# Kernel tuning notes

Measured on AMD Instinct MI355X. Metric: run time of the kernel, lower is better.

The kernel has to match this reference:

```python
import jax, jax.numpy as jnp
import numpy as np

BLOCK = 64  # block_size from config
NEG_INF = -1e9


def setup_inputs() -> dict:
    key = jax.random.key(0)
    k1, k2, k3, k4 = jax.random.split(key, 4)
    B, H, S, D = 2, 8, 2048, 64
    nb = S // BLOCK  # 32 blocks per side
    query = jax.random.normal(k1, (B, H, S, D), dtype=jnp.float32)
    key_t = jax.random.normal(k2, (B, H, S, D), dtype=jnp.float32)
    value = jax.random.normal(k3, (B, H, S, D), dtype=jnp.float32)
    # binary block mask; force diagonal blocks on so every row has >=1 valid key
    mat = jax.random.randint(k4, (nb, nb), 0, 2).astype(jnp.int32)
    mat = mat.at[jnp.arange(nb), jnp.arange(nb)].set(1)
    mask = jnp.ones((B, S), dtype=jnp.float32)  # padding mask (1 = keep)
    return {"query": query, "key": key_t, "value": value, "mask": mask, "mat": mat}


def reference(query, key, value, mask, mat):
    # Upsample block mask [nb, nb] -> dense [S, S] (nearest, like nn.Upsample)
    block_dense = jnp.repeat(jnp.repeat(mat, BLOCK, axis=0), BLOCK, axis=1) > 0
    # Block-sparse QK^T: only positions inside nonzero blocks participate.
    scores = jnp.einsum('bhqd,bhkd->bhqk', query, key)
    # Additive padding-mask bias, as in the original: 1e6 * (1 - mask)
    scores = scores - 1e6 * (1.0 - mask)[:, None, None, :]
    # Positions outside the block pattern are excluded from the softmax.
    scores = jnp.where(block_dense[None, None, :, :], scores, NEG_INF)
    attn = jax.nn.softmax(scores, axis=-1)
    out = jnp.einsum('bhqk,bhkd->bhqd', attn, value)
    return out
```

## Files before the change

### kernel.cpp

```cpp
#include <hip/hip_runtime.h>


typedef __attribute__((ext_vector_type(8))) short short8;
typedef __attribute__((ext_vector_type(4))) short short4_;
typedef __attribute__((ext_vector_type(4))) float float4_;

#define B_   2
#define H_   8
#define S_   2048
#define D_   64
#define NB_  32
#define KP   72

__device__ __forceinline__ short f2bf(float f) {
    union { float f; unsigned int u; } x; x.f = f;
    unsigned int r = x.u + 0x7FFFu + ((x.u >> 16) & 1u);
    return (short)(r >> 16);
}
__device__ __forceinline__ float bf2f(short s) {
    union { unsigned int u; float f; } x; x.u = ((unsigned int)(unsigned short)s) << 16;
    return x.f;
}

__global__ __launch_bounds__(256)
void preconvert_kernel(const float* __restrict__ K, const float* __restrict__ V,
                       short* __restrict__ Khi, short* __restrict__ Klo,
                       short* __restrict__ Vt) {
    __shared__ short vn[64 * KP];
    const int tid = threadIdx.x;
    const int kt  = blockIdx.x;
    const int bh  = blockIdx.y;
    const size_t tb = ((size_t)bh * S_ + kt * 64) * D_;

#pragma unroll
    for (int it = 0; it < 4; ++it) {
        int i = tid + it * 256;
        int row = i >> 4, c4 = (i & 15) * 4;
        float4_ kv = *(const float4_*)(K + tb + row * D_ + c4);
        short4_ hi, lo;
#pragma unroll
        for (int e = 0; e < 4; ++e) {
            hi[e] = f2bf(kv[e]);
            lo[e] = f2bf(kv[e] - bf2f(hi[e]));
        }
        *(short4_*)(Khi + tb + row * D_ + c4) = hi;
        *(short4_*)(Klo + tb + row * D_ + c4) = lo;
        float4_ vv = *(const float4_*)(V + tb + row * D_ + c4);
        short4_ vb;
#pragma unroll
        for (int e = 0; e < 4; ++e) vb[e] = f2bf(vv[e]);
        *(short4_*)&vn[row * KP + c4] = vb;
    }
    __syncthreads();
#pragma unroll
    for (int it = 0; it < 2; ++it) {
        int i = tid + it * 256;
        int rowd = i >> 3, key8 = (i & 7) * 8;
        short8 o;
#pragma unroll
        for (int e = 0; e < 8; ++e) o[e] = vn[(key8 + e) * KP + rowd];
        *(short8*)(Vt + ((size_t)bh * D_ + rowd) * S_ + kt * 64 + key8) = o;
    }
}

__global__ __launch_bounds__(256, 2)
void blockmask_attn_mfma(const float* __restrict__ Q,
                         const float* __restrict__ K,
                         const float* __restrict__ V,
                         const float* __restrict__ Msk,
                         const int* __restrict__ Mat,
                         float* __restrict__ O,
                         const short* __restrict__ Khi_g,
                         const short* __restrict__ Klo_g,
                         const short* __restrict__ Vt_g,
                         int use_pre) {
    __shared__ __align__(16) short lds[4 * 64 * KP];
    short* Khi = lds;
    short* Klo = lds + 64 * KP;
    short* Vt  = lds + 2 * 64 * KP;
    short* Pl  = lds + 3 * 64 * KP;

    const int tid  = threadIdx.x;
    const int wave = tid >> 6;
    const int lane = tid & 63;
    const int c    = lane & 15;
    const int quad = lane >> 4;

    const int qb = blockIdx.x;
    const int bh = blockIdx.y;
    const int b  = bh / H_;
    const size_t base = (size_t)bh * S_ * D_;

    short8 qh0, qh1, ql0, ql1;
    {
        const float* qp = Q + base + (size_t)(qb * 64 + wave * 16 + c) * D_ + quad * 8;
#pragma unroll
        for (int e = 0; e < 8; ++e) {
            float f0 = qp[e], f1 = qp[e + 32];
            qh0[e] = f2bf(f0); ql0[e] = f2bf(f0 - bf2f(qh0[e]));
            qh1[e] = f2bf(f1); ql1[e] = f2bf(f1 - bf2f(qh1[e]));
        }
    }

    float4_ o[4];
    float l_part[4];
#pragma unroll
    for (int t = 0; t < 4; ++t) { o[t][0] = 0.f; o[t][1] = 0.f; o[t][2] = 0.f; o[t][3] = 0.f; }
#pragma unroll
    for (int j = 0; j < 4; ++j) l_part[j] = 0.f;

    for (int kb = 0; kb < NB_; ++kb) {
        if (Mat[qb * NB_ + kb] == 0) continue;

        __syncthreads();
        if (use_pre) {
            const short* kh = Khi_g + base + (size_t)kb * 64 * D_;
            const short* kl = Klo_g + base + (size_t)kb * 64 * D_;
            const short* vt = Vt_g + (size_t)bh * D_ * S_ + kb * 64;
#pragma unroll
            for (int it = 0; it < 2; ++it) {
                int i = tid + it * 256;
                int row = i >> 3, col8 = (i & 7) * 8;
                *(short8*)&Khi[row * KP + col8] = *(const short8*)(kh + row * D_ + col8);
                *(short8*)&Klo[row * KP + col8] = *(const short8*)(kl + row * D_ + col8);
                *(short8*)&Vt[row * KP + col8]  = *(const short8*)(vt + (size_t)row * S_ + col8);
            }
        } else {
            const float* kg = K + base + (size_t)kb * 64 * D_;
            const float* vg = V + base + (size_t)kb * 64 * D_;
#pragma unroll
            for (int it = 0; it < 4; ++it) {
                int i = tid + it * 256;
                int row = i >> 4, c4 = (i & 15) * 4;
                float4_ kv = *(const float4_*)(kg + row * D_ + c4);
                short4_ hi, lo;
#pragma unroll
                for (int e = 0; e < 4; ++e) {
                    hi[e] = f2bf(kv[e]);
                    lo[e] = f2bf(kv[e] - bf2f(hi[e]));
                }
                *(short4_*)&Khi[row * KP + c4] = hi;
                *(short4_*)&Klo[row * KP + c4] = lo;
                float4_ vv = *(const float4_*)(vg + row * D_ + c4);
#pragma unroll
                for (int e = 0; e < 4; ++e) Vt[(c4 + e) * KP + row] = f2bf(vv[e]);
            }
        }
        __syncthreads();

        float4_ sc[4];
#pragma unroll
        for (int t = 0; t < 4; ++t) { sc[t][0] = 0.f; sc[t][1] = 0.f; sc[t][2] = 0.f; sc[t][3] = 0.f; }
#pragma unroll
        for (int t = 0; t < 4; ++t) {
            const short* kph = &Khi[(t * 16 + c) * KP + quad * 8];
            const short* kpl = &Klo[(t * 16 + c) * KP + quad * 8];
            short8 kh0 = *(const short8*)(kph);
            short8 kh1 = *(const short8*)(kph + 32);
            short8 kl0 = *(const short8*)(kpl);
            short8 kl1 = *(const short8*)(kpl + 32);
            sc[t] = __builtin_amdgcn_mfma_f32_16x16x32_bf16(qh0, kh0, sc[t], 0, 0, 0);
            sc[t] = __builtin_amdgcn_mfma_f32_16x16x32_bf16(qh1, kh1, sc[t], 0, 0, 0);
            sc[t] = __builtin_amdgcn_mfma_f32_16x16x32_bf16(qh0, kl0, sc[t], 0, 0, 0);
            sc[t] = __builtin_amdgcn_mfma_f32_16x16x32_bf16(qh1, kl1, sc[t], 0, 0, 0);
            sc[t] = __builtin_amdgcn_mfma_f32_16x16x32_bf16(ql0, kh0, sc[t], 0, 0, 0);
            sc[t] = __builtin_amdgcn_mfma_f32_16x16x32_bf16(ql1, kh1, sc[t], 0, 0, 0);
        }

        short* Pw = Pl + wave * 16 * KP;
#pragma unroll
        for (int t = 0; t < 4; ++t) {
            float bias = -1.0e6f * (1.0f - Msk[(size_t)b * S_ + kb * 64 + t * 16 + c]);
#pragma unroll
            for (int j = 0; j < 4; ++j) {
                float p = __expf(sc[t][j] + bias);
                l_part[j] += p;
                Pw[(quad * 4 + j) * KP + t * 16 + c] = f2bf(p);
            }
        }

        const short* pp = Pl + wave * 16 * KP + c * KP + quad * 8;
        short8 pa0 = *(const short8*)(pp);
        short8 pa1 = *(const short8*)(pp + 32);

#pragma unroll
        for (int t = 0; t < 4; ++t) {
            const short* vp = &Vt[(t * 16 + c) * KP + quad * 8];
            short8 vb0 = *(const short8*)(vp);
            short8 vb1 = *(const short8*)(vp + 32);
            o[t] = __builtin_amdgcn_mfma_f32_16x16x32_bf16(pa0, vb0, o[t], 0, 0, 0);
            o[t] = __builtin_amdgcn_mfma_f32_16x16x32_bf16(pa1, vb1, o[t], 0, 0, 0);
        }
    }

#pragma unroll
    for (int j = 0; j < 4; ++j) {
        float rs = l_part[j];
        rs += __shfl_xor(rs, 1);
        rs += __shfl_xor(rs, 2);
        rs += __shfl_xor(rs, 4);
        rs += __shfl_xor(rs, 8);
        float inv = 1.0f / rs;
        size_t rowoff = base + (size_t)(qb * 64 + wave * 16 + quad * 4 + j) * D_;
#pragma unroll
        for (int t = 0; t < 4; ++t)
            O[rowoff + t * 16 + c] = o[t][j] * inv;
    }
}

extern "C" void kernel_launch(void* const* d_in, const int* in_sizes, int n_in,
                              void* d_out, int out_size, void* d_ws, size_t ws_size,
                              hipStream_t stream) {
    const float* q   = (const float*)d_in[0];
    const float* k   = (const float*)d_in[1];
    const float* v   = (const float*)d_in[2];
    const float* msk = (const float*)d_in[3];
    const int*   mat = (const int*)d_in[4];
    float*       out = (float*)d_out;

    const size_t elems = (size_t)B_ * H_ * S_ * D_;
    const size_t need  = 3 * elems * sizeof(short);
    int use_pre = (ws_size >= need) ? 1 : 0;

    short* khi = (short*)d_ws;
    short* klo = khi + elems;
    short* vt  = klo + elems;

    dim3 grid(NB_, B_ * H_);
    dim3 block(256);
    if (use_pre)
        preconvert_kernel<<<grid, block, 0, stream>>>(k, v, khi, klo, vt);
    blockmask_attn_mfma<<<grid, block, 0, stream>>>(q, k, v, msk, mat, out,
                                                    khi, klo, vt, use_pre);
}
```

Baseline: 124.9 us.

## Use one-wave blocks loading K/V fragments directly from global, skipping LDS staging

Adds a new attention kernel where each 64-thread block handles 16 query rows and loads K-hi/K-lo/V-transposed fragments straight from global memory into registers, with no LDS staging and no block barriers. It also stores V transposed per 64-key tile so each tile is contiguous, and walks the nonzero blocks with a ballot bitmask instead of testing every block. This removes the __syncthreads and LDS copy overhead and raises block count, but the same K/V data is now fetched from global (through cache) by four times as many blocks, raising cache traffic and register pressure.

```diff
diff --git a/kernel.cpp b/kernel.cpp
--- a/kernel.cpp
+++ b/kernel.cpp
@@ -25,7 +25,7 @@
 __global__ __launch_bounds__(256)
 void preconvert_kernel(const float* __restrict__ K, const float* __restrict__ V,
                        short* __restrict__ Khi, short* __restrict__ Klo,
-                       short* __restrict__ Vt) {
+                       short* __restrict__ Vtb) {
     __shared__ short vn[64 * KP];
     const int tid = threadIdx.x;
     const int kt  = blockIdx.x;
@@ -59,21 +59,129 @@
         short8 o;
 #pragma unroll
         for (int e = 0; e < 8; ++e) o[e] = vn[(key8 + e) * KP + rowd];
-        *(short8*)(Vt + ((size_t)bh * D_ + rowd) * S_ + kt * 64 + key8) = o;
+        *(short8*)(Vtb + (((size_t)(bh * NB_ + kt)) * 64 + rowd) * 64 + key8) = o;
+    }
+}
+
+__global__ __launch_bounds__(64, 2)
+void attn_mfma_nb(const float* __restrict__ Q,
+                  const float* __restrict__ Msk,
+                  const int* __restrict__ Mat,
+                  float* __restrict__ O,
+                  const short* __restrict__ Khi_g,
+                  const short* __restrict__ Klo_g,
+                  const short* __restrict__ Vtb_g) {
+    __shared__ __align__(16) short Pl[16 * KP];
+
+    const int lane = threadIdx.x & 63;
+    const int c    = lane & 15;
+    const int quad = lane >> 4;
+
+    const int qt = blockIdx.x;
+    const int bh = blockIdx.y;
+    const int b  = bh / H_;
+    const int qb = qt >> 2;
+    const size_t base = (size_t)bh * S_ * D_;
+
+    short8 qh0, qh1, ql0, ql1;
+    {
+        const float* qp = Q + base + (size_t)(qt * 16 + c) * D_ + quad * 8;
+#pragma unroll
+        for (int e = 0; e < 8; ++e) {
+            float f0 = qp[e], f1 = qp[e + 32];
+            qh0[e] = f2bf(f0); ql0[e] = f2bf(f0 - bf2f(qh0[e]));
+            qh1[e] = f2bf(f1); ql1[e] = f2bf(f1 - bf2f(qh1[e]));
+        }
+    }
+
+    float4_ o[4];
+    float l_part[4];
+#pragma unroll
+    for (int t = 0; t < 4; ++t) { o[t][0] = 0.f; o[t][1] = 0.f; o[t][2] = 0.f; o[t][3] = 0.f; }
+#pragma unroll
+    for (int j = 0; j < 4; ++j) l_part[j] = 0.f;
+
+    unsigned long long bm = __ballot(Mat[qb * NB_ + (lane & 31)] != 0);
+    unsigned int mbits = (unsigned int)(bm & 0xFFFFFFFFull);
+
+    while (mbits) {
+        const int kb = __builtin_ctz(mbits);
+        mbits &= mbits - 1;
+
+        const short* kh = Khi_g + base + (size_t)kb * 64 * D_;
+        const short* kl = Klo_g + base + (size_t)kb * 64 * D_;
+        const short* vt = Vtb_g + ((size_t)(bh * NB_ + kb)) * 64 * 64;
+
+        short8 KH0[4], KH1[4], KL0[4], KL1[4], VB0[4], VB1[4];
+        float biasv[4];
+#pragma unroll
+        for (int t = 0; t < 4; ++t) {
+            const int off = (t * 16 + c) * 64 + quad * 8;
+            VB0[t] = *(const short8*)(vt + off);
+            VB1[t] = *(const short8*)(vt + off + 32);
+            KH0[t] = *(const short8*)(kh + off);
+            KH1[t] = *(const short8*)(kh + off + 32);
+            KL0[t] = *(const short8*)(kl + off);
+            KL1[t] = *(const short8*)(kl + off + 32);
+            biasv[t] = -1.0e6f * (1.0f - Msk[(size_t)b * S_ + kb * 64 + t * 16 + c]);
+        }
+
+        float4_ sc[4];
+#pragma unroll
+        for (int t = 0; t < 4; ++t) { sc[t][0] = 0.f; sc[t][1] = 0.f; sc[t][2] = 0.f; sc[t][3] = 0.f; }
+#pragma unroll
+        for (int t = 0; t < 4; ++t) {
+            sc[t] = __builtin_amdgcn_mfma_f32_16x16x32_bf16(qh0, KH0[t], sc[t], 0, 0, 0);
+            sc[t] = __builtin_amdgcn_mfma_f32_16x16x32_bf16(qh1, KH1[t], sc[t], 0, 0, 0);
+            sc[t] = __builtin_amdgcn_mfma_f32_16x16x32_bf16(qh0, KL0[t], sc[t], 0, 0, 0);
+            sc[t] = __builtin_amdgcn_mfma_f32_16x16x32_bf16(qh1, KL1[t], sc[t], 0, 0, 0);
+            sc[t] = __builtin_amdgcn_mfma_f32_16x16x32_bf16(ql0, KH0[t], sc[t], 0, 0, 0);
+            sc[t] = __builtin_amdgcn_mfma_f32_16x16x32_bf16(ql1, KH1[t], sc[t], 0, 0, 0);
+        }
+
+#pragma unroll
+        for (int t = 0; t < 4; ++t) {
+#pragma unroll
+            for (int j = 0; j < 4; ++j) {
+                float p = __expf(sc[t][j] + biasv[t]);
+                l_part[j] += p;
+                Pl[(quad * 4 + j) * KP + t * 16 + c] = f2bf(p);
+            }
+        }
+
+        const short* pp = Pl + c * KP + quad * 8;
+        short8 pa0 = *(const short8*)(pp);
+        short8 pa1 = *(const short8*)(pp + 32);
+
+#pragma unroll
+        for (int t = 0; t < 4; ++t) {
+            o[t] = __builtin_amdgcn_mfma_f32_16x16x32_bf16(pa0, VB0[t], o[t], 0, 0, 0);
+            o[t] = __builtin_amdgcn_mfma_f32_16x16x32_bf16(pa1, VB1[t], o[t], 0, 0, 0);
+        }
+    }
+
+#pragma unroll
+    for (int j = 0; j < 4; ++j) {
+        float rs = l_part[j];
+        rs += __shfl_xor(rs, 1);
+        rs += __shfl_xor(rs, 2);
+        rs += __shfl_xor(rs, 4);
+        rs += __shfl_xor(rs, 8);
+        float inv = 1.0f / rs;
+        size_t rowoff = base + (size_t)(qt * 16 + quad * 4 + j) * D_;
+#pragma unroll
+        for (int t = 0; t < 4; ++t)
+            O[rowoff + t * 16 + c] = o[t][j] * inv;
     }
 }
 
 __global__ __launch_bounds__(256, 2)
-void blockmask_attn_mfma(const float* __restrict__ Q,
-                         const float* __restrict__ K,
-                         const float* __restrict__ V,
-                         const float* __restrict__ Msk,
-                         const int* __restrict__ Mat,
-                         float* __restrict__ O,
-                         const short* __restrict__ Khi_g,
-                         const short* __restrict__ Klo_g,
-                         const short* __restrict__ Vt_g,
-                         int use_pre) {
+void attn_mfma_fb(const float* __restrict__ Q,
+                  const float* __restrict__ K,
+                  const float* __restrict__ V,
+                  const float* __restrict__ Msk,
+                  const int* __restrict__ Mat,
+                  float* __restrict__ O) {
     __shared__ __align__(16) short lds[4 * 64 * KP];
     short* Khi = lds;
     short* Klo = lds + 64 * KP;
@@ -113,19 +221,7 @@
         if (Mat[qb * NB_ + kb] == 0) continue;
 
         __syncthreads();
-        if (use_pre) {
-            const short* kh = Khi_g + base + (size_t)kb * 64 * D_;
-            const short* kl = Klo_g + base + (size_t)kb * 64 * D_;
-            const short* vt = Vt_g + (size_t)bh * D_ * S_ + kb * 64;
-#pragma unroll
-            for (int it = 0; it < 2; ++it) {
-                int i = tid + it * 256;
-                int row = i >> 3, col8 = (i & 7) * 8;
-                *(short8*)&Khi[row * KP + col8] = *(const short8*)(kh + row * D_ + col8);
-                *(short8*)&Klo[row * KP + col8] = *(const short8*)(kl + row * D_ + col8);
-                *(short8*)&Vt[row * KP + col8]  = *(const short8*)(vt + (size_t)row * S_ + col8);
-            }
-        } else {
+        {
             const float* kg = K + base + (size_t)kb * 64 * D_;
             const float* vg = V + base + (size_t)kb * 64 * D_;
 #pragma unroll
@@ -220,16 +316,19 @@
 
     const size_t elems = (size_t)B_ * H_ * S_ * D_;
     const size_t need  = 3 * elems * sizeof(short);
-    int use_pre = (ws_size >= need) ? 1 : 0;
+    const int use_pre  = (ws_size >= need) ? 1 : 0;
 
     short* khi = (short*)d_ws;
     short* klo = khi + elems;
-    short* vt  = klo + elems;
-
-    dim3 grid(NB_, B_ * H_);
-    dim3 block(256);
-    if (use_pre)
-        preconvert_kernel<<<grid, block, 0, stream>>>(k, v, khi, klo, vt);
-    blockmask_attn_mfma<<<grid, block, 0, stream>>>(q, k, v, msk, mat, out,
-                                                    khi, klo, vt, use_pre);
-}
+    short* vtb = klo + elems;
+
+    if (use_pre) {
+        dim3 pgrid(NB_, B_ * H_);
+        preconvert_kernel<<<pgrid, dim3(256), 0, stream>>>(k, v, khi, klo, vtb);
+        dim3 grid(S_ / 16, B_ * H_);
+        attn_mfma_nb<<<grid, dim3(64), 0, stream>>>(q, msk, mat, out, khi, klo, vtb);
+    } else {
+        dim3 grid(NB_, B_ * H_);
+        attn_mfma_fb<<<grid, dim3(256), 0, stream>>>(q, k, v, msk, mat, out);
+    }
+}
```

New measurement: 202.9 us. 62.5% more time.
